# Optimization experiments

Hardware: AMD Instinct MI355X
Metric: run time of the kernel (lower is better)

The kernel has to match this reference:

```python
import jax, jax.numpy as jnp
import numpy as np

B, D, H, K = 8192, 1280, 16384, 64


def setup_inputs() -> dict:
    key = jax.random.key(0)
    k1, k2, k3 = jax.random.split(key, 3)
    x = jax.random.normal(k1, (B, D), dtype=jnp.float32)
    # encoder weight [hidden_dim, input_dim] (torch Linear layout)
    W_enc = jax.random.normal(k2, (H, D), dtype=jnp.float32) * (1.0 / np.sqrt(D))
    b_enc = jnp.zeros((H,), dtype=jnp.float32)
    # decoder weight [input_dim, hidden_dim], unit-norm columns scaled by 0.1
    W_dec = jax.random.normal(k3, (D, H), dtype=jnp.float32)
    W_dec = 0.1 * W_dec / jnp.linalg.norm(W_dec, axis=0, keepdims=True)
    b_dec = jnp.zeros((D,), dtype=jnp.float32)
    b_pre = jnp.zeros((D,), dtype=jnp.float32)
    return {"x": x, "W_enc": W_enc, "b_enc": b_enc, "W_dec": W_dec,
            "b_dec": b_dec, "b_pre": b_pre, "k": K}


def reference(x, W_enc, b_enc, W_dec, b_dec, b_pre, k):
    # --- encode ---
    x_centered = x - b_pre                                   # [B, D]
    pre = jnp.einsum('bd,hd->bh', x_centered, W_enc) + b_enc  # [B, H]
    vals, idx = jax.lax.top_k(pre, k)                        # [B, k]
    rows = jnp.arange(pre.shape[0])[:, None]                 # [B, 1]
    hidden = jnp.zeros_like(pre).at[rows, idx].set(jax.nn.relu(vals))  # [B, H]
    # --- decode ---
    reconstructed = jnp.einsum('bh,dh->bd', hidden, W_dec) + b_dec + b_pre
    # --- losses ---
    reconstruction_loss = jnp.mean((reconstructed - x) ** 2)
    l0 = jnp.mean(jnp.sum((hidden > 0).astype(jnp.float32), axis=-1))
    sparsity_loss = jnp.array(0.0, dtype=jnp.float32)
    loss = reconstruction_loss
    return reconstructed, hidden, loss, reconstruction_loss, sparsity_loss, l0
```

## Files before the change

kernel.cpp:

```cpp
#include <hip/hip_runtime.h>
#include <hip/hip_bf16.h>

constexpr int K_MAX    = 128;
constexpr int S_MAX    = 128;
constexpr int A_MAX    = 256;
constexpr int CAND_MAX = 512;
constexpr int BM = 128, BN = 128, BKF = 16;
constexpr int NBITER = 42;
constexpr int D_MAX   = 2048;
constexpr int H_FIX   = 16384;

typedef __attribute__((ext_vector_type(8))) short bf16x8;
typedef __attribute__((ext_vector_type(8))) unsigned short u16x8;
typedef __attribute__((ext_vector_type(4))) float f32x4;

__device__ inline unsigned short f2bf(float f) {
  unsigned u = __float_as_uint(f);
  return (unsigned short)((u + 0x7fff + ((u >> 16) & 1)) >> 16);
}
__device__ inline unsigned short key_of(float f) {
  unsigned short b = f2bf(f);
  return b ^ ((b & 0x8000) ? 0xFFFF : 0x8000);
}
__device__ inline float val_of_key(unsigned short kk) {
  unsigned short b = (kk & 0x8000) ? (unsigned short)(kk ^ 0x8000)
                                   : (unsigned short)(kk ^ 0xFFFF);
  return __uint_as_float(((unsigned)b) << 16);
}
__device__ inline float bf2f(unsigned short b) {
  return __uint_as_float(((unsigned)b) << 16);
}

__device__ inline int lds_slot(int r, int c) {
  return ((r >> 1) << 4) | ((r & 1) << 3) | (c ^ ((r >> 1) & 7));
}

__global__ __launch_bounds__(256) void prep_xb(
    const float* __restrict__ x, const float* __restrict__ b_pre,
    unsigned short* __restrict__ Xb, int D, size_t total4)
{
  for (size_t i = blockIdx.x * 256 + threadIdx.x; i < total4; i += (size_t)gridDim.x * 256) {
    const size_t e = i * 4;
    const int d = (int)(e % D);
    float4 xv = *reinterpret_cast<const float4*>(x + e);
    float4 bp = *reinterpret_cast<const float4*>(b_pre + d);
    ushort4 o;
    o.x = f2bf(xv.x - bp.x); o.y = f2bf(xv.y - bp.y);
    o.z = f2bf(xv.z - bp.z); o.w = f2bf(xv.w - bp.w);
    *reinterpret_cast<ushort4*>(Xb + e) = o;
  }
}

__global__ __launch_bounds__(256) void prep_wb(
    const float* __restrict__ W, unsigned short* __restrict__ Wb, size_t total4)
{
  for (size_t i = blockIdx.x * 256 + threadIdx.x; i < total4; i += (size_t)gridDim.x * 256) {
    const size_t e = i * 4;
    float4 wv = *reinterpret_cast<const float4*>(W + e);
    ushort4 o;
    o.x = f2bf(wv.x); o.y = f2bf(wv.y); o.z = f2bf(wv.z); o.w = f2bf(wv.w);
    *reinterpret_cast<ushort4*>(Wb + e) = o;
  }
}

__global__ __launch_bounds__(512, 2) void enc_gemm_bf16(
    const unsigned short* __restrict__ Xb, const unsigned short* __restrict__ Wb,
    const float* __restrict__ b_enc, float* __restrict__ pre, int D, int H)
{
  __shared__ unsigned short As[2][2048 * 8];
  __shared__ unsigned short Bs[2][2048 * 8];
  const int tid  = threadIdx.x;
  const int wave = tid >> 6, lane = tid & 63;
  const int m0 = blockIdx.y * 256, n0 = blockIdx.x * 256;
  const int wm = (wave >> 1) * 64;
  const int wn = (wave & 1) * 128;
  const int l16 = lane & 15, lhi = lane >> 4;

  f32x4 acc[4][8];
#pragma unroll
  for (int i = 0; i < 4; ++i)
#pragma unroll
    for (int j = 0; j < 8; ++j) acc[i][j] = (f32x4){0.f, 0.f, 0.f, 0.f};

  const int NT = D / 64;

  auto stageA = [&](int buf, int h, int kb) {
#pragma unroll
    for (int i = 0; i < 2; ++i) {
      const int idx = i * 512 + wave * 64 + lane;
      const int sr = idx >> 4, u = idx & 15;
      const int r  = (sr << 1) | (u >> 3);
      const int ch = (u & 7) ^ (sr & 7);
      __builtin_amdgcn_global_load_lds(
          (const __attribute__((address_space(1))) unsigned int*)
              (Xb + (size_t)(m0 + h * 128 + r) * D + kb + ch * 8),
          (__attribute__((address_space(3))) unsigned int*)
              (&As[buf][(size_t)(h * 1024 + idx) * 8]), 16, 0, 0);
    }
  };
  auto stageBq = [&](int buf, int q, int kb) {
    const int s  = (q & 1) * 512 + wave * 64 + lane;
    const int sr = s >> 4, u = s & 15;
    const int r  = (sr << 1) | (u >> 3);
    const int ch = (u & 7) ^ (sr & 7);
    __builtin_amdgcn_global_load_lds(
        (const __attribute__((address_space(1))) unsigned int*)
            (Wb + (size_t)(n0 + (q >> 1) * 128 + r) * D + kb + ch * 8),
        (__attribute__((address_space(3))) unsigned int*)
            (&Bs[buf][(size_t)((q >> 1) * 1024 + s) * 8]), 16, 0, 0);
  };
  auto readA = [&](int buf, int mi, int kk) -> bf16x8 {
    const int gr = wm + mi * 16 + l16;
    return *reinterpret_cast<const bf16x8*>(
        &As[buf][(size_t)((gr >> 7) * 1024 + lds_slot(gr & 127, kk * 4 + lhi)) * 8]);
  };
  auto readB = [&](int buf, int ni, int kk) -> bf16x8 {
    const int gr = wn + ni * 16 + l16;
    return *reinterpret_cast<const bf16x8*>(
        &Bs[buf][(size_t)((gr >> 7) * 1024 + lds_slot(gr & 127, kk * 4 + lhi)) * 8]);
  };

  stageA(0, 0, 0); stageA(0, 1, 0);
  stageBq(0, 0, 0); stageBq(0, 2, 0);
  stageBq(0, 1, 0); stageBq(0, 3, 0);

  int cur = 0;
  for (int t = 0; t < NT; ++t) {
    const int nxt = cur ^ 1;
    const int kb1 = (t + 1) * 64;
    const bool more = (t + 1 < NT);

    bf16x8 af[4][2], bf[2][2];

    asm volatile("s_waitcnt vmcnt(2)" ::: "memory");
    __builtin_amdgcn_s_barrier();
#pragma unroll
    for (int mi = 0; mi < 4; ++mi)
#pragma unroll
      for (int kk = 0; kk < 2; ++kk) af[mi][kk] = readA(cur, mi, kk);
#pragma unroll
    for (int j = 0; j < 2; ++j)
#pragma unroll
      for (int kk = 0; kk < 2; ++kk) bf[j][kk] = readB(cur, j, kk);
    if (more) stageA(nxt, 0, kb1);
    __builtin_amdgcn_s_setprio(1);
#pragma unroll
    for (int mi = 0; mi < 4; ++mi)
#pragma unroll
      for (int j = 0; j < 2; ++j)
#pragma unroll
        for (int kk = 0; kk < 2; ++kk)
          acc[mi][j] = __builtin_amdgcn_mfma_f32_16x16x32_bf16(af[mi][kk], bf[j][kk], acc[mi][j], 0, 0, 0);
    __builtin_amdgcn_s_setprio(0);

#pragma unroll
    for (int j = 0; j < 2; ++j)
#pragma unroll
      for (int kk = 0; kk < 2; ++kk) bf[j][kk] = readB(cur, 2 + j, kk);
    if (more) stageA(nxt, 1, kb1);
    __builtin_amdgcn_s_setprio(1);
#pragma unroll
    for (int mi = 0; mi < 4; ++mi)
#pragma unroll
      for (int j = 0; j < 2; ++j)
#pragma unroll
        for (int kk = 0; kk < 2; ++kk)
          acc[mi][2 + j] = __builtin_amdgcn_mfma_f32_16x16x32_bf16(af[mi][kk], bf[j][kk], acc[mi][2 + j], 0, 0, 0);
    __builtin_amdgcn_s_setprio(0);

    if (more) { asm volatile("s_waitcnt vmcnt(4)" ::: "memory"); }
    else      { asm volatile("s_waitcnt vmcnt(0)" ::: "memory"); }
    __builtin_amdgcn_s_barrier();
#pragma unroll
    for (int j = 0; j < 2; ++j)
#pragma unroll
      for (int kk = 0; kk < 2; ++kk) bf[j][kk] = readB(cur, 4 + j, kk);
    if (more) { stageBq(nxt, 0, kb1); stageBq(nxt, 2, kb1); }
    __builtin_amdgcn_s_setprio(1);
#pragma unroll
    for (int mi = 0; mi < 4; ++mi)
#pragma unroll
      for (int j = 0; j < 2; ++j)
#pragma unroll
        for (int kk = 0; kk < 2; ++kk)
          acc[mi][4 + j] = __builtin_amdgcn_mfma_f32_16x16x32_bf16(af[mi][kk], bf[j][kk], acc[mi][4 + j], 0, 0, 0);
    __builtin_amdgcn_s_setprio(0);

#pragma unroll
    for (int j = 0; j < 2; ++j)
#pragma unroll
      for (int kk = 0; kk < 2; ++kk) bf[j][kk] = readB(cur, 6 + j, kk);
    if (more) { stageBq(nxt, 1, kb1); stageBq(nxt, 3, kb1); }
    __builtin_amdgcn_s_setprio(1);
#pragma unroll
    for (int mi = 0; mi < 4; ++mi)
#pragma unroll
      for (int j = 0; j < 2; ++j)
#pragma unroll
        for (int kk = 0; kk < 2; ++kk)
          acc[mi][6 + j] = __builtin_amdgcn_mfma_f32_16x16x32_bf16(af[mi][kk], bf[j][kk], acc[mi][6 + j], 0, 0, 0);
    __builtin_amdgcn_s_setprio(0);

    cur = nxt;
  }

#pragma unroll
  for (int ni = 0; ni < 8; ++ni) {
    const int n = n0 + wn + ni * 16 + l16;
    const float be = b_enc[n];
#pragma unroll
    for (int mi = 0; mi < 4; ++mi) {
      const int mbase = m0 + wm + mi * 16 + lhi * 4;
#pragma unroll
      for (int r = 0; r < 4; ++r) {
        unsigned short* prow = (unsigned short*)(pre + (size_t)(mbase + r) * H);
        prow[n] = key_of(acc[mi][ni][r] + be);
      }
    }
  }
}

__global__ __launch_bounds__(256) void topk_classify_keys(
    float* __restrict__ hidden,
    int* __restrict__ sure_ix, float* __restrict__ sure_val, int* __restrict__ sure_cnt,
    int* __restrict__ amb_ix, int* __restrict__ amb_cnt,
    const int* __restrict__ kptr, float delta)
{
  constexpr int H = H_FIX, NC = H_FIX / (256 * 8);
  __shared__ int hist[4096];
  __shared__ int chunk[256];
  __shared__ int misc[8];

  const int tid = threadIdx.x, b = blockIdx.x;
  const int k = min(*kptr, K_MAX);
  float* hrow = hidden + (size_t)b * H;
  const unsigned short* krow = (const unsigned short*)hrow;

  if (tid < 8) misc[tid] = 0;
  for (int i = tid; i < 4096; i += 256) hist[i] = 0;

  u16x8 kv[NC];
#pragma unroll
  for (int i = 0; i < NC; ++i)
    kv[i] = *reinterpret_cast<const u16x8*>(krow + ((size_t)i * 256 + tid) * 8);
  __syncthreads();

  const float4 z4 = {0.f, 0.f, 0.f, 0.f};
  for (int i = tid; i < (H >> 2); i += 256)
    reinterpret_cast<float4*>(hrow)[i] = z4;

#pragma unroll
  for (int i = 0; i < NC; ++i)
#pragma unroll
    for (int j = 0; j < 8; ++j)
      atomicAdd(&hist[((unsigned)(unsigned short)kv[i][j]) >> 4], 1);
  __syncthreads();

  int csum = 0;
#pragma unroll
  for (int j = 0; j < 16; ++j) csum += hist[tid * 16 + j];
  chunk[tid] = csum;
  __syncthreads();
  int gt = 0;
  for (int j = tid + 1; j < 256; ++j) gt += chunk[j];
  {
    int run = gt;
#pragma unroll
    for (int j = 15; j >= 0; --j) {
      const int hc = hist[tid * 16 + j];
      if (run < k && k <= run + hc) { misc[0] = tid * 16 + j; misc[1] = run; }
      run += hc;
    }
  }
  __syncthreads();
  const int b1 = misc[0];
  if (tid < 16) chunk[tid] = 0;
  __syncthreads();
#pragma unroll
  for (int i = 0; i < NC; ++i)
#pragma unroll
    for (int j = 0; j < 8; ++j) {
      const unsigned kk = (unsigned)(unsigned short)kv[i][j];
      if ((int)(kk >> 4) == b1) atomicAdd(&chunk[kk & 15], 1);
    }
  __syncthreads();
  if (tid == 0) {
    int run = misc[1];
    int K16 = b1 << 4;
    for (int j = 15; j >= 0; --j) {
      const int c = chunk[j];
      if (run < k && k <= run + c) K16 = (b1 << 4) | j;
      run += c;
    }
    const float v_lo = val_of_key((unsigned short)K16);
    const float v_hi = val_of_key((unsigned short)min(K16 + 1, 65535));
    const float ulp = v_hi - v_lo;
    const float vs = v_hi + delta;
    const float va = v_lo - ulp - delta;
    int ks = key_of(vs); if (val_of_key((unsigned short)ks) > vs) --ks;
    int ka = key_of(va); if (val_of_key((unsigned short)ka) < va) ++ka;
    misc[2] = ks; misc[3] = ka;
  }
  __syncthreads();
  const unsigned ks = (unsigned)misc[2], ka = (unsigned)misc[3];

#pragma unroll
  for (int i = 0; i < NC; ++i)
#pragma unroll
    for (int j = 0; j < 8; ++j) {
      const unsigned kk = (unsigned)(unsigned short)kv[i][j];
      if (kk > ks) {
        const int p = atomicAdd(&misc[4], 1);
        if (p < S_MAX) {
          const int h = (i * 256 + tid) * 8 + j;
          sure_ix[(size_t)b * S_MAX + p] = h;
          sure_val[(size_t)b * S_MAX + p] = val_of_key((unsigned short)kk);
        }
      } else if (kk >= ka) {
        const int p = atomicAdd(&misc[5], 1);
        if (p < A_MAX) amb_ix[(size_t)b * A_MAX + p] = (i * 256 + tid) * 8 + j;
      }
    }
  __syncthreads();
  if (tid == 0) {
    sure_cnt[b] = min(misc[4], S_MAX);
    amb_cnt[b]  = min(misc[5], A_MAX);
  }
}

__global__ __launch_bounds__(256) void refine_scatter(
    const float* __restrict__ X, const float* __restrict__ b_pre,
    const float* __restrict__ W, const float* __restrict__ b_enc,
    const int* __restrict__ sure_ix, const float* __restrict__ sure_val,
    const int* __restrict__ sure_cnt,
    const int* __restrict__ amb_ix, const int* __restrict__ amb_cnt,
    const int* __restrict__ kptr,
    float* __restrict__ hidden, int* __restrict__ tk_idx, float* __restrict__ tk_val, int D)
{
  constexpr int H = H_FIX;
  __shared__ float  xr[D_MAX];
  __shared__ double asv[A_MAX];
  __shared__ int    aix[A_MAX];
  const int tid = threadIdx.x, b = blockIdx.x;
  const int k = min(*kptr, K_MAX);
  const int S = min(min(sure_cnt[b], S_MAX), k);
  const int A = min(amb_cnt[b], A_MAX);
  float* hrow = hidden + (size_t)b * H;

  for (int d = tid; d < D; d += 256) xr[d] = X[(size_t)b * D + d] - b_pre[d];
  for (int c = tid; c < A; c += 256) aix[c] = amb_ix[(size_t)b * A_MAX + c];

  for (int i = tid; i < S; i += 256) {
    const int h = sure_ix[(size_t)b * S_MAX + i];
    const float v = sure_val[(size_t)b * S_MAX + i];
    const float rv = (v > 0.f) ? v : 0.f;
    hrow[h] = rv;
    tk_idx[(size_t)b * K_MAX + i] = h;
    tk_val[(size_t)b * K_MAX + i] = rv;
  }
  __syncthreads();

  const int wid = tid >> 6, lane = tid & 63;
  for (int c = wid; c < A; c += 4) {
    const int h = aix[c];
    const float* wr = W + (size_t)h * D;
    double s0 = 0.0, s1 = 0.0;
    int i = lane;
    for (; i + 64 < D; i += 128) {
      s0 += (double)xr[i] * (double)wr[i];
      s1 += (double)xr[i + 64] * (double)wr[i + 64];
    }
    if (i < D) s0 += (double)xr[i] * (double)wr[i];
    double s = s0 + s1;
    for (int off = 32; off; off >>= 1) s += __shfl_xor(s, off);
    if (lane == 0) asv[c] = s + (double)b_enc[h];
  }
  __syncthreads();

  const int m = k - S;
  for (int c = tid; c < A; c += 256) {
    const double v = asv[c];
    const int h = aix[c];
    int r = 0;
    for (int j = 0; j < A; ++j) {
      const double vj = asv[j];
      r += ((vj > v) || (vj == v && aix[j] < h)) ? 1 : 0;
    }
    if (r < m) {
      const float rv = (v > 0.0) ? (float)v : 0.f;
      hrow[h] = rv;
      tk_idx[(size_t)b * K_MAX + S + r] = h;
      tk_val[(size_t)b * K_MAX + S + r] = rv;
    }
  }
}

__global__ __launch_bounds__(256) void enc_gemm_f32(
    const float* __restrict__ X, const float* __restrict__ W,
    const float* __restrict__ b_enc, const float* __restrict__ b_pre,
    float* __restrict__ pre, int D, int H)
{
  __shared__ float As[BKF][BM + 4];
  __shared__ float Bs[BKF][BN + 4];
  const int tid = threadIdx.x;
  const int m0 = blockIdx.y * BM;
  const int n0 = blockIdx.x * BN;
  const int tx = tid & 15, ty = tid >> 4;
  float acc[8][8];
#pragma unroll
  for (int i = 0; i < 8; ++i)
#pragma unroll
    for (int j = 0; j < 8; ++j) acc[i][j] = 0.f;

  for (int kb = 0; kb < D; kb += BKF) {
#pragma unroll
    for (int t = 0; t < 2; ++t) {
      const int f4i = tid + t * 256;
      const int row = f4i >> 2;
      const int kq  = (f4i & 3) << 2;
      float4 xv = *reinterpret_cast<const float4*>(X + (size_t)(m0 + row) * D + kb + kq);
      float4 bp = *reinterpret_cast<const float4*>(b_pre + kb + kq);
      As[kq + 0][row] = xv.x - bp.x; As[kq + 1][row] = xv.y - bp.y;
      As[kq + 2][row] = xv.z - bp.z; As[kq + 3][row] = xv.w - bp.w;
      float4 wv = *reinterpret_cast<const float4*>(W + (size_t)(n0 + row) * D + kb + kq);
      Bs[kq + 0][row] = wv.x; Bs[kq + 1][row] = wv.y;
      Bs[kq + 2][row] = wv.z; Bs[kq + 3][row] = wv.w;
    }
    __syncthreads();
#pragma unroll
    for (int kk = 0; kk < BKF; ++kk) {
      float4 a0 = *reinterpret_cast<const float4*>(&As[kk][ty * 8]);
      float4 a1 = *reinterpret_cast<const float4*>(&As[kk][ty * 8 + 4]);
      float4 b0 = *reinterpret_cast<const float4*>(&Bs[kk][tx * 8]);
      float4 b1 = *reinterpret_cast<const float4*>(&Bs[kk][tx * 8 + 4]);
      float av[8] = {a0.x, a0.y, a0.z, a0.w, a1.x, a1.y, a1.z, a1.w};
      float bv[8] = {b0.x, b0.y, b0.z, b0.w, b1.x, b1.y, b1.z, b1.w};
#pragma unroll
      for (int i = 0; i < 8; ++i)
#pragma unroll
        for (int j = 0; j < 8; ++j) acc[i][j] += av[i] * bv[j];
    }
    __syncthreads();
  }
#pragma unroll
  for (int i = 0; i < 8; ++i) {
    const size_t m = (size_t)(m0 + ty * 8 + i);
#pragma unroll
    for (int j = 0; j < 8; j += 4) {
      const int n = n0 + tx * 8 + j;
      float4 o;
      o.x = acc[i][j + 0] + b_enc[n + 0];
      o.y = acc[i][j + 1] + b_enc[n + 1];
      o.z = acc[i][j + 2] + b_enc[n + 2];
      o.w = acc[i][j + 3] + b_enc[n + 3];
      *reinterpret_cast<float4*>(pre + m * H + n) = o;
    }
  }
}

__global__ __launch_bounds__(256) void topk_refine(
    const float* __restrict__ X, const float* __restrict__ b_pre,
    const float* __restrict__ W, const float* __restrict__ b_enc,
    float* __restrict__ hidden, int* __restrict__ tk_idx, float* __restrict__ tk_val,
    const int* __restrict__ kptr, int D, int H, float margin)
{
  extern __shared__ char smem_raw[];
  double* cand_val = reinterpret_cast<double*>(smem_raw);
  float*  xr       = reinterpret_cast<float*>(cand_val + CAND_MAX);
  int*    cand_idx = reinterpret_cast<int*>(xr + D);
  int*    misc     = cand_idx + CAND_MAX;

  const int tid = threadIdx.x;
  const int b = blockIdx.x;
  const int k = min(*kptr, K_MAX);
  float* hrow = hidden + (size_t)b * H;

  for (int i = tid; i < NBITER + 2; i += 256) misc[i] = 0;
  for (int d = tid; d < D; d += 256) xr[d] = X[(size_t)b * D + d] - b_pre[d];

  float f[64];
#pragma unroll
  for (int i = 0; i < 16; ++i) {
    const int base = i * 1024 + tid * 4;
    float4 v = {-3e38f, -3e38f, -3e38f, -3e38f};
    if (base + 3 < H) v = *reinterpret_cast<const float4*>(hrow + base);
    f[4 * i + 0] = v.x; f[4 * i + 1] = v.y; f[4 * i + 2] = v.z; f[4 * i + 3] = v.w;
  }
  __syncthreads();

  float lo = -1e4f, hi = 1e4f;
  for (int it = 0; it < NBITER; ++it) {
    const float mid = 0.5f * (lo + hi);
    int cnt = 0;
#pragma unroll
    for (int j = 0; j < 64; ++j) cnt += (f[j] >= mid) ? 1 : 0;
    for (int off = 32; off; off >>= 1) cnt += __shfl_xor(cnt, off);
    if ((tid & 63) == 0) atomicAdd(&misc[it], cnt);
    __syncthreads();
    if (misc[it] >= k) lo = mid; else hi = mid;
  }

  const float thresh = lo - margin;
#pragma unroll
  for (int j = 0; j < 64; ++j) {
    if (f[j] >= thresh) {
      const int h = (j >> 2) * 1024 + tid * 4 + (j & 3);
      if (h < H) {
        int pos = atomicAdd(&misc[NBITER], 1);
        if (pos < CAND_MAX) cand_idx[pos] = h;
      }
    }
  }
  __syncthreads();
  const int C = min(misc[NBITER], CAND_MAX);

  const int wid = tid >> 6, lane = tid & 63;
  for (int c = wid; c < C; c += 4) {
    const int h = cand_idx[c];
    const float* wr = W + (size_t)h * D;
    double s = 0.0;
    for (int i = lane; i < D; i += 64) s += (double)xr[i] * (double)wr[i];
    for (int off = 32; off; off >>= 1) s += __shfl_xor(s, off);
    if (lane == 0) cand_val[c] = s + (double)b_enc[h];
  }
  __syncthreads();

  const float4 z4 = {0.f, 0.f, 0.f, 0.f};
  for (int i = tid; i < (H >> 2); i += 256)
    reinterpret_cast<float4*>(hrow)[i] = z4;
  __syncthreads();

  for (int c = tid; c < C; c += 256) {
    const double v = cand_val[c];
    const int h = cand_idx[c];
    int r = 0;
    for (int j = 0; j < C; ++j) {
      const double vj = cand_val[j];
      r += ((vj > v) || (vj == v && cand_idx[j] < h)) ? 1 : 0;
    }
    if (r < k) {
      const float rv = (v > 0.0) ? (float)v : 0.f;
      hrow[h] = rv;
      tk_idx[(size_t)b * K_MAX + r] = h;
      tk_val[(size_t)b * K_MAX + r] = rv;
    }
  }
}

__global__ __launch_bounds__(256) void transpose_wdec_bf16(
    const float* __restrict__ Wsrc, unsigned short* __restrict__ WT, int D, int H)
{
  __shared__ float tile[32][33];
  const int c  = threadIdx.x & 31;
  const int r0 = threadIdx.x >> 5;
  const int h0 = blockIdx.x * 32;
  const int d0 = blockIdx.y * 32;
#pragma unroll
  for (int r = r0; r < 32; r += 8) {
    const int d = d0 + r, h = h0 + c;
    if (d < D && h < H) tile[r][c] = Wsrc[(size_t)d * H + h];
  }
  __syncthreads();
#pragma unroll
  for (int r = r0; r < 32; r += 8) {
    const int h = h0 + r, d = d0 + c;
    if (h < H && d < D) WT[(size_t)h * D + d] = f2bf(tile[c][r]);
  }
}

__global__ __launch_bounds__(256) void decode_loss(
    const float* __restrict__ X, const float* __restrict__ b_pre,
    const float* __restrict__ b_dec, const float* __restrict__ Wfull,
    const unsigned short* __restrict__ WTb,
    const int* __restrict__ tk_idx, const float* __restrict__ tk_val,
    const int* __restrict__ kptr,
    float* __restrict__ recon, double* __restrict__ row_ssq,
    int D, int H, int useWT)
{
  __shared__ int   sidx[K_MAX];
  __shared__ float sval[K_MAX];
  __shared__ double sd[4];
  const int tid = threadIdx.x, b = blockIdx.x;
  const int k = min(*kptr, K_MAX);
  if (tid < k) {
    sidx[tid] = tk_idx[(size_t)b * K_MAX + tid];
    sval[tid] = tk_val[(size_t)b * K_MAX + tid];
  }
  __syncthreads();
  double ssq = 0.0;
  const int D4 = D >> 2;
  for (int dc = tid; dc < D4; dc += 256) {
    const int d = dc * 4;
    float4 bd = *reinterpret_cast<const float4*>(b_dec + d);
    float4 bp = *reinterpret_cast<const float4*>(b_pre + d);
    float4 a = {bd.x + bp.x, bd.y + bp.y, bd.z + bp.z, bd.w + bp.w};
    if (useWT) {
#pragma unroll 4
      for (int j = 0; j < k; ++j) {
        const ushort4 w = *reinterpret_cast<const ushort4*>(WTb + (size_t)sidx[j] * D + d);
        const float s = sval[j];
        a.x += s * bf2f(w.x); a.y += s * bf2f(w.y);
        a.z += s * bf2f(w.z); a.w += s * bf2f(w.w);
      }
    } else {
#pragma unroll 4
      for (int j = 0; j < k; ++j) {
        const float s = sval[j];
        const int h = sidx[j];
        a.x += s * Wfull[(size_t)(d + 0) * H + h];
        a.y += s * Wfull[(size_t)(d + 1) * H + h];
        a.z += s * Wfull[(size_t)(d + 2) * H + h];
        a.w += s * Wfull[(size_t)(d + 3) * H + h];
      }
    }
    *reinterpret_cast<float4*>(recon + (size_t)b * D + d) = a;
    float4 xv = *reinterpret_cast<const float4*>(X + (size_t)b * D + d);
    const double d0 = (double)a.x - (double)xv.x;
    const double d1 = (double)a.y - (double)xv.y;
    const double d2 = (double)a.z - (double)xv.z;
    const double d3 = (double)a.w - (double)xv.w;
    ssq += d0 * d0 + d1 * d1 + d2 * d2 + d3 * d3;
  }
  for (int off = 32; off; off >>= 1) ssq += __shfl_xor(ssq, off);
  if ((tid & 63) == 0) sd[tid >> 6] = ssq;
  __syncthreads();
  if (tid == 0) row_ssq[b] = sd[0] + sd[1] + sd[2] + sd[3];
}

__global__ __launch_bounds__(256) void finalize_part(
    const double* __restrict__ row_ssq, const float* __restrict__ tk_val,
    const int* __restrict__ kptr, double* __restrict__ part_s, int* __restrict__ part_c,
    int Bdim, int rows_per_blk)
{
  __shared__ double sd[4];
  __shared__ int si[4];
  const int tid = threadIdx.x;
  const int k = min(*kptr, K_MAX);
  const int b0 = blockIdx.x * rows_per_blk;
  const int b1 = min(b0 + rows_per_blk, Bdim);
  double s = 0.0;
  for (int i = b0 + tid; i < b1; i += 256) s += row_ssq[i];
  int cnt = 0;
  const int total = (b1 - b0) * k;
  for (int i = tid; i < total; i += 256) {
    const int bb = b0 + i / k, j = i - (i / k) * k;
    cnt += (tk_val[(size_t)bb * K_MAX + j] > 0.f) ? 1 : 0;
  }
  for (int off = 32; off; off >>= 1) { s += __shfl_xor(s, off); cnt += __shfl_xor(cnt, off); }
  if ((tid & 63) == 0) { sd[tid >> 6] = s; si[tid >> 6] = cnt; }
  __syncthreads();
  if (tid == 0) {
    part_s[blockIdx.x] = sd[0] + sd[1] + sd[2] + sd[3];
    part_c[blockIdx.x] = si[0] + si[1] + si[2] + si[3];
  }
}

__global__ __launch_bounds__(64) void finalize_k2(
    const double* __restrict__ part_s, const int* __restrict__ part_c,
    float* __restrict__ scalars, int nparts, int Bdim, int D)
{
  const int tid = threadIdx.x;
  double s = (tid < nparts) ? part_s[tid] : 0.0;
  int cnt = (tid < nparts) ? part_c[tid] : 0;
  for (int off = 32; off; off >>= 1) { s += __shfl_xor(s, off); cnt += __shfl_xor(cnt, off); }
  if (tid == 0) {
    const double rl = s / ((double)Bdim * (double)D);
    scalars[0] = (float)rl;
    scalars[1] = (float)rl;
    scalars[2] = 0.f;
    scalars[3] = (float)((double)cnt / Bdim);
  }
}

extern "C" void kernel_launch(void* const* d_in, const int* in_sizes, int n_in,
                              void* d_out, int out_size, void* d_ws, size_t ws_size,
                              hipStream_t stream)
{
  const float* x     = (const float*)d_in[0];
  const float* W_enc = (const float*)d_in[1];
  const float* b_enc = (const float*)d_in[2];
  const float* W_dec = (const float*)d_in[3];
  const float* b_dec = (const float*)d_in[4];
  const float* b_pre = (const float*)d_in[5];
  const int*   kptr  = (const int*)d_in[6];

  const int D = in_sizes[4];
  const int H = in_sizes[2];
  const int B = in_sizes[0] / D;

  float* recon   = (float*)d_out;
  float* hidden  = recon + (size_t)B * D;
  float* scalars = hidden + (size_t)B * H;

  size_t off = 0;
  int* tk_idx = (int*)((char*)d_ws + off);        off += (size_t)B * K_MAX * sizeof(int);
  float* tk_val = (float*)((char*)d_ws + off);    off += (size_t)B * K_MAX * sizeof(float);
  off = (off + 7) & ~(size_t)7;
  double* row_ssq = (double*)((char*)d_ws + off); off += (size_t)B * sizeof(double);
  double* part_s = (double*)((char*)d_ws + off);  off += 64 * sizeof(double);
  int* part_c = (int*)((char*)d_ws + off);        off += 64 * sizeof(int);
  off = (off + 7) & ~(size_t)7;

  unsigned short* Xb = (unsigned short*)((char*)d_ws + off);
  off += (size_t)B * D * sizeof(unsigned short);
  unsigned short* Wb = (unsigned short*)((char*)d_ws + off);
  off += (size_t)H * D * sizeof(unsigned short);
  const int useBF16 = (off <= ws_size) ? 1 : 0;

  unsigned short* WTb = (unsigned short*)((char*)d_ws + off);
  off += (size_t)D * H * sizeof(unsigned short);
  const int useWT = (off <= ws_size) ? 1 : 0;

  int* sure_ix = (int*)((char*)d_ws + off);       off += (size_t)B * S_MAX * sizeof(int);
  float* sure_val = (float*)((char*)d_ws + off);  off += (size_t)B * S_MAX * sizeof(float);
  int* sure_cnt = (int*)((char*)d_ws + off);      off += (size_t)B * sizeof(int);
  int* amb_ix = (int*)((char*)d_ws + off);        off += (size_t)B * A_MAX * sizeof(int);
  int* amb_cnt = (int*)((char*)d_ws + off);       off += (size_t)B * sizeof(int);
  off = (off + 7) & ~(size_t)7;
  const int useSPLIT = (useBF16 && off <= ws_size) ? 1 : 0;

  const bool fast_ok = (D % 64 == 0) && (D <= D_MAX) &&
                       (H == H_FIX) && (B % 256 == 0);

  if (useBF16 && fast_ok && useSPLIT) {
    const size_t tx4 = (size_t)B * D / 4, tw4 = (size_t)H * D / 4;
    prep_xb<<<2048, 256, 0, stream>>>(x, b_pre, Xb, D, tx4);
    prep_wb<<<2048, 256, 0, stream>>>(W_enc, Wb, tw4);
    dim3 gg(H / 256, B / 256);
    enc_gemm_bf16<<<gg, 512, 0, stream>>>(Xb, Wb, b_enc, hidden, D, H);
    topk_classify_keys<<<B, 256, 0, stream>>>(hidden, sure_ix, sure_val, sure_cnt,
                                              amb_ix, amb_cnt, kptr, 0.05f);
    refine_scatter<<<B, 256, 0, stream>>>(x, b_pre, W_enc, b_enc,
                                          sure_ix, sure_val, sure_cnt,
                                          amb_ix, amb_cnt, kptr,
                                          hidden, tk_idx, tk_val, D);
  } else {
    dim3 gg(H / BN, B / BM);
    enc_gemm_f32<<<gg, 256, 0, stream>>>(x, W_enc, b_enc, b_pre, hidden, D, H);
    const size_t sh = CAND_MAX * sizeof(double) + (size_t)D * sizeof(float)
                    + CAND_MAX * sizeof(int) + (NBITER + 8) * sizeof(int);
    topk_refine<<<B, 256, sh, stream>>>(x, b_pre, W_enc, b_enc, hidden,
                                        tk_idx, tk_val, kptr, D, H, 1e-3f);
  }

  if (useWT)
    transpose_wdec_bf16<<<dim3((H + 31) / 32, (D + 31) / 32), 256, 0, stream>>>(W_dec, WTb, D, H);

  decode_loss<<<B, 256, 0, stream>>>(x, b_pre, b_dec, W_dec, WTb,
                                     tk_idx, tk_val, kptr, recon, row_ssq, D, H, useWT);

  const int rpb = (B + 63) / 64;
  finalize_part<<<64, 256, 0, stream>>>(row_ssq, tk_val, kptr, part_s, part_c, B, rpb);
  finalize_k2<<<1, 64, 0, stream>>>(part_s, part_c, scalars, 64, B, D);
}
```

Before: 994.5 us.

## Fuse top-k classify and refine kernels; widen decode to two rows per block

```diff
diff --git a/kernel.cpp b/kernel.cpp
--- a/kernel.cpp
+++ b/kernel.cpp
@@ -2,7 +2,6 @@
 #include <hip/hip_bf16.h>
 
 constexpr int K_MAX    = 128;
-constexpr int S_MAX    = 128;
 constexpr int A_MAX    = 256;
 constexpr int CAND_MAX = 512;
 constexpr int BM = 128, BN = 128, BKF = 16;
@@ -220,16 +219,19 @@
   }
 }
 
-__global__ __launch_bounds__(256) void topk_classify_keys(
-    float* __restrict__ hidden,
-    int* __restrict__ sure_ix, float* __restrict__ sure_val, int* __restrict__ sure_cnt,
-    int* __restrict__ amb_ix, int* __restrict__ amb_cnt,
-    const int* __restrict__ kptr, float delta)
+__global__ __launch_bounds__(256) void select_refine(
+    const float* __restrict__ X, const float* __restrict__ b_pre,
+    const float* __restrict__ W, const float* __restrict__ b_enc,
+    float* __restrict__ hidden, int* __restrict__ tk_idx, float* __restrict__ tk_val,
+    const int* __restrict__ kptr, int D, float delta)
 {
   constexpr int H = H_FIX, NC = H_FIX / (256 * 8);
-  __shared__ int hist[4096];
-  __shared__ int chunk[256];
-  __shared__ int misc[8];
+  __shared__ int    hist[4096];
+  __shared__ int    chunk[256];
+  __shared__ int    misc[8];
+  __shared__ float  xr[D_MAX];
+  __shared__ double asv[A_MAX];
+  __shared__ int    aix[A_MAX];
 
   const int tid = threadIdx.x, b = blockIdx.x;
   const int k = min(*kptr, K_MAX);
@@ -248,6 +250,7 @@
   const float4 z4 = {0.f, 0.f, 0.f, 0.f};
   for (int i = tid; i < (H >> 2); i += 256)
     reinterpret_cast<float4*>(hrow)[i] = z4;
+  for (int d = tid; d < D; d += 256) xr[d] = X[(size_t)b * D + d] - b_pre[d];
 
 #pragma unroll
   for (int i = 0; i < NC; ++i)
@@ -311,54 +314,22 @@
       const unsigned kk = (unsigned)(unsigned short)kv[i][j];
       if (kk > ks) {
         const int p = atomicAdd(&misc[4], 1);
-        if (p < S_MAX) {
+        if (p < k) {
           const int h = (i * 256 + tid) * 8 + j;
-          sure_ix[(size_t)b * S_MAX + p] = h;
-          sure_val[(size_t)b * S_MAX + p] = val_of_key((unsigned short)kk);
+          const float v = val_of_key((unsigned short)kk);
+          const float rv = (v > 0.f) ? v : 0.f;
+          hrow[h] = rv;
+          tk_idx[(size_t)b * K_MAX + p] = h;
+          tk_val[(size_t)b * K_MAX + p] = rv;
         }
       } else if (kk >= ka) {
         const int p = atomicAdd(&misc[5], 1);
-        if (p < A_MAX) amb_ix[(size_t)b * A_MAX + p] = (i * 256 + tid) * 8 + j;
+        if (p < A_MAX) aix[p] = (i * 256 + tid) * 8 + j;
       }
     }
   __syncthreads();
-  if (tid == 0) {
-    sure_cnt[b] = min(misc[4], S_MAX);
-    amb_cnt[b]  = min(misc[5], A_MAX);
-  }
-}
-
-__global__ __launch_bounds__(256) void refine_scatter(
-    const float* __restrict__ X, const float* __restrict__ b_pre,
-    const float* __restrict__ W, const float* __restrict__ b_enc,
-    const int* __restrict__ sure_ix, const float* __restrict__ sure_val,
-    const int* __restrict__ sure_cnt,
-    const int* __restrict__ amb_ix, const int* __restrict__ amb_cnt,
-    const int* __restrict__ kptr,
-    float* __restrict__ hidden, int* __restrict__ tk_idx, float* __restrict__ tk_val, int D)
-{
-  constexpr int H = H_FIX;
-  __shared__ float  xr[D_MAX];
-  __shared__ double asv[A_MAX];
-  __shared__ int    aix[A_MAX];
-  const int tid = threadIdx.x, b = blockIdx.x;
-  const int k = min(*kptr, K_MAX);
-  const int S = min(min(sure_cnt[b], S_MAX), k);
-  const int A = min(amb_cnt[b], A_MAX);
-  float* hrow = hidden + (size_t)b * H;
-
-  for (int d = tid; d < D; d += 256) xr[d] = X[(size_t)b * D + d] - b_pre[d];
-  for (int c = tid; c < A; c += 256) aix[c] = amb_ix[(size_t)b * A_MAX + c];
-
-  for (int i = tid; i < S; i += 256) {
-    const int h = sure_ix[(size_t)b * S_MAX + i];
-    const float v = sure_val[(size_t)b * S_MAX + i];
-    const float rv = (v > 0.f) ? v : 0.f;
-    hrow[h] = rv;
-    tk_idx[(size_t)b * K_MAX + i] = h;
-    tk_val[(size_t)b * K_MAX + i] = rv;
-  }
-  __syncthreads();
+  const int S = min(misc[4], k);
+  const int A = min(misc[5], A_MAX);
 
   const int wid = tid >> 6, lane = tid & 63;
   for (int c = wid; c < A; c += 4) {
@@ -568,14 +539,69 @@
   }
 }
 
+__global__ __launch_bounds__(256) void decode_loss2(
+    const float* __restrict__ X, const float* __restrict__ b_pre,
+    const float* __restrict__ b_dec, const unsigned short* __restrict__ WTb,
+    const int* __restrict__ tk_idx, const float* __restrict__ tk_val,
+    const int* __restrict__ kptr,
+    float* __restrict__ recon, double* __restrict__ row_ssq, int D)
+{
+  __shared__ int   sidx[2][K_MAX];
+  __shared__ float sval[2][K_MAX];
+  __shared__ double sd[4];
+  const int tid = threadIdx.x;
+  const int half = tid >> 7, lt = tid & 127;
+  const int b = blockIdx.x * 2 + half;
+  const int k = min(*kptr, K_MAX);
+  if (lt < k) {
+    sidx[half][lt] = tk_idx[(size_t)b * K_MAX + lt];
+    sval[half][lt] = tk_val[(size_t)b * K_MAX + lt];
+  }
+  __syncthreads();
+
+  double ssq = 0.0;
+  const int D8 = D >> 3;
+  for (int dc = lt; dc < D8; dc += 128) {
+    const int d = dc * 8;
+    float a[8];
+#pragma unroll
+    for (int q = 0; q < 2; ++q) {
+      float4 bd = *reinterpret_cast<const float4*>(b_dec + d + q * 4);
+      float4 bp = *reinterpret_cast<const float4*>(b_pre + d + q * 4);
+      a[q * 4 + 0] = bd.x + bp.x; a[q * 4 + 1] = bd.y + bp.y;
+      a[q * 4 + 2] = bd.z + bp.z; a[q * 4 + 3] = bd.w + bp.w;
+    }
+#pragma unroll 4
+    for (int j = 0; j < k; ++j) {
+      const u16x8 w = *reinterpret_cast<const u16x8*>(WTb + (size_t)sidx[half][j] * D + d);
+      const float s = sval[half][j];
+#pragma unroll
+      for (int e = 0; e < 8; ++e) a[e] += s * bf2f((unsigned short)w[e]);
+    }
+#pragma unroll
+    for (int q = 0; q < 2; ++q) {
+      float4 o = {a[q * 4 + 0], a[q * 4 + 1], a[q * 4 + 2], a[q * 4 + 3]};
+      *reinterpret_cast<float4*>(recon + (size_t)b * D + d + q * 4) = o;
+    }
+#pragma unroll
+    for (int e = 0; e < 8; ++e) {
+      const double df = (double)a[e] - (double)X[(size_t)b * D + d + e];
+      ssq += df * df;
+    }
+  }
+  for (int off = 32; off; off >>= 1) ssq += __shfl_xor(ssq, off);
+  if ((tid & 63) == 0) sd[tid >> 6] = ssq;
+  __syncthreads();
+  if (tid == 0) row_ssq[blockIdx.x * 2 + 0] = sd[0] + sd[1];
+  if (tid == 128) row_ssq[blockIdx.x * 2 + 1] = sd[2] + sd[3];
+}
+
 __global__ __launch_bounds__(256) void decode_loss(
     const float* __restrict__ X, const float* __restrict__ b_pre,
     const float* __restrict__ b_dec, const float* __restrict__ Wfull,
-    const unsigned short* __restrict__ WTb,
     const int* __restrict__ tk_idx, const float* __restrict__ tk_val,
     const int* __restrict__ kptr,
-    float* __restrict__ recon, double* __restrict__ row_ssq,
-    int D, int H, int useWT)
+    float* __restrict__ recon, double* __restrict__ row_ssq, int D, int H)
 {
   __shared__ int   sidx[K_MAX];
   __shared__ float sval[K_MAX];
@@ -588,38 +614,13 @@
   }
   __syncthreads();
   double ssq = 0.0;
-  const int D4 = D >> 2;
-  for (int dc = tid; dc < D4; dc += 256) {
-    const int d = dc * 4;
-    float4 bd = *reinterpret_cast<const float4*>(b_dec + d);
-    float4 bp = *reinterpret_cast<const float4*>(b_pre + d);
-    float4 a = {bd.x + bp.x, bd.y + bp.y, bd.z + bp.z, bd.w + bp.w};
-    if (useWT) {
+  for (int d = tid; d < D; d += 256) {
+    float a = b_dec[d] + b_pre[d];
 #pragma unroll 4
-      for (int j = 0; j < k; ++j) {
-        const ushort4 w = *reinterpret_cast<const ushort4*>(WTb + (size_t)sidx[j] * D + d);
-        const float s = sval[j];
-        a.x += s * bf2f(w.x); a.y += s * bf2f(w.y);
-        a.z += s * bf2f(w.z); a.w += s * bf2f(w.w);
-      }
-    } else {
-#pragma unroll 4
-      for (int j = 0; j < k; ++j) {
-        const float s = sval[j];
-        const int h = sidx[j];
-        a.x += s * Wfull[(size_t)(d + 0) * H + h];
-        a.y += s * Wfull[(size_t)(d + 1) * H + h];
-        a.z += s * Wfull[(size_t)(d + 2) * H + h];
-        a.w += s * Wfull[(size_t)(d + 3) * H + h];
-      }
-    }
-    *reinterpret_cast<float4*>(recon + (size_t)b * D + d) = a;
-    float4 xv = *reinterpret_cast<const float4*>(X + (size_t)b * D + d);
-    const double d0 = (double)a.x - (double)xv.x;
-    const double d1 = (double)a.y - (double)xv.y;
-    const double d2 = (double)a.z - (double)xv.z;
-    const double d3 = (double)a.w - (double)xv.w;
-    ssq += d0 * d0 + d1 * d1 + d2 * d2 + d3 * d3;
+    for (int j = 0; j < k; ++j) a += sval[j] * Wfull[(size_t)d * H + sidx[j]];
+    recon[(size_t)b * D + d] = a;
+    const double diff = (double)a - (double)X[(size_t)b * D + d];
+    ssq += diff * diff;
   }
   for (int off = 32; off; off >>= 1) ssq += __shfl_xor(ssq, off);
   if ((tid & 63) == 0) sd[tid >> 6] = ssq;
@@ -705,35 +706,24 @@
   off += (size_t)B * D * sizeof(unsigned short);
   unsigned short* Wb = (unsigned short*)((char*)d_ws + off);
   off += (size_t)H * D * sizeof(unsigned short);
-  const int useBF16 = (off <= ws_size) ? 1 : 0;
-
   unsigned short* WTb = (unsigned short*)((char*)d_ws + off);
   off += (size_t)D * H * sizeof(unsigned short);
-  const int useWT = (off <= ws_size) ? 1 : 0;
-
-  int* sure_ix = (int*)((char*)d_ws + off);       off += (size_t)B * S_MAX * sizeof(int);
-  float* sure_val = (float*)((char*)d_ws + off);  off += (size_t)B * S_MAX * sizeof(float);
-  int* sure_cnt = (int*)((char*)d_ws + off);      off += (size_t)B * sizeof(int);
-  int* amb_ix = (int*)((char*)d_ws + off);        off += (size_t)B * A_MAX * sizeof(int);
-  int* amb_cnt = (int*)((char*)d_ws + off);       off += (size_t)B * sizeof(int);
-  off = (off + 7) & ~(size_t)7;
-  const int useSPLIT = (useBF16 && off <= ws_size) ? 1 : 0;
-
-  const bool fast_ok = (D % 64 == 0) && (D <= D_MAX) &&
+  const int useFAST = (off <= ws_size) ? 1 : 0;
+
+  const bool fast_ok = (D % 64 == 0) && (D % 8 == 0) && (D <= D_MAX) &&
                        (H == H_FIX) && (B % 256 == 0);
 
-  if (useBF16 && fast_ok && useSPLIT) {
+  if (useFAST && fast_ok) {
     const size_t tx4 = (size_t)B * D / 4, tw4 = (size_t)H * D / 4;
     prep_xb<<<2048, 256, 0, stream>>>(x, b_pre, Xb, D, tx4);
     prep_wb<<<2048, 256, 0, stream>>>(W_enc, Wb, tw4);
     dim3 gg(H / 256, B / 256);
     enc_gemm_bf16<<<gg, 512, 0, stream>>>(Xb, Wb, b_enc, hidden, D, H);
-    topk_classify_keys<<<B, 256, 0, stream>>>(hidden, sure_ix, sure_val, sure_cnt,
-                                              amb_ix, amb_cnt, kptr, 0.05f);
-    refine_scatter<<<B, 256, 0, stream>>>(x, b_pre, W_enc, b_enc,
-                                          sure_ix, sure_val, sure_cnt,
-                                          amb_ix, amb_cnt, kptr,
-                                          hidden, tk_idx, tk_val, D);
+    select_refine<<<B, 256, 0, stream>>>(x, b_pre, W_enc, b_enc, hidden,
+                                         tk_idx, tk_val, kptr, D, 0.05f);
+    transpose_wdec_bf16<<<dim3((H + 31) / 32, (D + 31) / 32), 256, 0, stream>>>(W_dec, WTb, D, H);
+    decode_loss2<<<B / 2, 256, 0, stream>>>(x, b_pre, b_dec, WTb,
+                                            tk_idx, tk_val, kptr, recon, row_ssq, D);
   } else {
     dim3 gg(H / BN, B / BM);
     enc_gemm_f32<<<gg, 256, 0, stream>>>(x, W_enc, b_enc, b_pre, hidden, D, H);
@@ -741,13 +731,9 @@
                     + CAND_MAX * sizeof(int) + (NBITER + 8) * sizeof(int);
     topk_refine<<<B, 256, sh, stream>>>(x, b_pre, W_enc, b_enc, hidden,
                                         tk_idx, tk_val, kptr, D, H, 1e-3f);
-  }
-
-  if (useWT)
-    transpose_wdec_bf16<<<dim3((H + 31) / 32, (D + 31) / 32), 256, 0, stream>>>(W_dec, WTb, D, H);
-
-  decode_loss<<<B, 256, 0, stream>>>(x, b_pre, b_dec, W_dec, WTb,
-                                     tk_idx, tk_val, kptr, recon, row_ssq, D, H, useWT);
+    decode_loss<<<B, 256, 0, stream>>>(x, b_pre, b_dec, W_dec,
+                                       tk_idx, tk_val, kptr, recon, row_ssq, D, H);
+  }
 
   const int rpb = (B + 63) / 64;
   finalize_part<<<64, 256, 0, stream>>>(row_ssq, tk_val, kptr, part_s, part_c, B, rpb);
```

After: 1.052 ms. +5.8%, slower.
